# Kernel optimization log

Measured on AMD Instinct MI355X. Metric: run time of the kernel, lower is better.

The kernel has to match this reference:

```python
import jax, jax.numpy as jnp
import numpy as np

SL, BS, HS, FFN, E, TOPK = 2048, 4, 1024, 4096, 8, 2
T = SL * BS

def setup_inputs() -> dict:
    key = jax.random.key(0)
    k1, k2, k3, k4, k5, k6 = jax.random.split(key, 6)
    x = jax.random.normal(k1, (SL, BS, HS), dtype=jnp.float32)
    expert_weights = jax.random.uniform(k2, (T, TOPK), dtype=jnp.float32)
    expert_indices = jax.random.randint(k3, (T, TOPK), 0, E).astype(jnp.int64)
    scores = jax.random.uniform(k4, (T, TOPK), dtype=jnp.float32)
    w1 = jax.random.normal(k5, (E, HS, FFN), dtype=jnp.float32) * 0.02
    w2 = jax.random.normal(k6, (E, FFN, HS), dtype=jnp.float32) * 0.02
    return {"x": x, "expert_weights": expert_weights, "scores": scores,
            "w1": w1, "w2": w2, "expert_indices": expert_indices}

def reference(x, expert_weights, scores, w1, w2, expert_indices):
    # Dropless MoE dispatch-compute-combine with router_type=None.
    # Math identity: megablocks gather/grouped-GEMM/scatter with per-copy
    # expert_weights equals, for each token t:
    #   out[t] = sum_k expert_weights[t,k] * MLP_{e(t,k)}(x[t])
    # We fold the top-k copies into a per-(token, expert) combine weight and
    # run one GEMM pair per expert (fixed small E), matching the grouped GEMM.
    sl, bs, hs = x.shape
    num_experts = w1.shape[0]
    xf = x.reshape(-1, hs)  # [T, hs]
    onehot = jax.nn.one_hot(expert_indices, num_experts, dtype=x.dtype)  # [T, k, E]
    combine = jnp.einsum("tk,tke->et", expert_weights, onehot)  # [E, T]

    def expert_step(acc, inputs):
        w1e, w2e, cw = inputs  # [hs, ffn], [ffn, hs], [T]
        h = jax.nn.gelu(xf @ w1e, approximate=False)  # [T, ffn]
        acc = acc + cw[:, None] * (h @ w2e)  # [T, hs]
        return acc, None

    out, _ = jax.lax.scan(expert_step, jnp.zeros_like(xf), (w1, w2, combine))
    return out.reshape(sl, bs, hs)
```

## Files before the change

### kernel.cpp

```cpp
#include <hip/hip_runtime.h>
#include <hip/hip_bf16.h>
#include <math.h>
#include <stdint.h>

#define N_TOK   8192
#define HS      1024
#define FFN     4096
#define NE      8
#define NA      16384
#define CAP     16384
#define BM      256
#define MAXT    72

typedef __attribute__((ext_vector_type(8))) short          bf16x8;
typedef __attribute__((ext_vector_type(4))) float          f32x4;
typedef __attribute__((ext_vector_type(4))) float          fvec4;
typedef __attribute__((ext_vector_type(4))) unsigned short usvec4;

__device__ __forceinline__ void gl_lds16(const void* g, void* l) {
  __builtin_amdgcn_global_load_lds(
      (const __attribute__((address_space(1))) unsigned int*)g,
      (__attribute__((address_space(3))) unsigned int*)l,
      16, 0, 0);
}

__device__ __forceinline__ unsigned short f2bf(float f) {
  union { float f; unsigned int u; } v; v.f = f;
  unsigned int r = v.u + 0x7FFFu + ((v.u >> 16) & 1u);
  return (unsigned short)(r >> 16);
}


__global__ void cvt_x_kernel(const fvec4* __restrict__ in, unsigned short* __restrict__ out, int n4) {
  int i = blockIdx.x * 256 + threadIdx.x;
  if (i >= n4) return;
  fvec4 v = in[i];
  usvec4 o;
  o[0] = f2bf(v[0]); o[1] = f2bf(v[1]); o[2] = f2bf(v[2]); o[3] = f2bf(v[3]);
  *(usvec4*)(out + (size_t)i * 4) = o;
}

__global__ void tpose_cvt_kernel(const float* __restrict__ in, unsigned short* __restrict__ out,
                                 int R, int C) {
  __shared__ float t[64][65];
  int bc = blockIdx.x * 64, br = blockIdx.y * 64, e = blockIdx.z;
  const float* ine = in + (size_t)e * R * C;
  unsigned short* oute = out + (size_t)e * R * C;
  int tx = threadIdx.x & 63, ty = threadIdx.x >> 6;
#pragma unroll
  for (int q = 0; q < 16; ++q) {
    int r = ty * 16 + q;
    t[r][tx] = ine[(size_t)(br + r) * C + bc + tx];
  }
  __syncthreads();
#pragma unroll
  for (int q = 0; q < 16; ++q) {
    int c = ty * 16 + q;
    oute[(size_t)(bc + c) * R + br + tx] = f2bf(t[tx][c]);
  }
}


__global__ void route_kernel(const int* __restrict__ idx, const float* __restrict__ wts,
                             int* __restrict__ counts, int* __restrict__ btok,
                             int* __restrict__ bslot, float* __restrict__ bw) {
  int a = blockIdx.x * 256 + threadIdx.x;
  if (a >= NA) return;
  int e = idx[a];
  int pos = atomicAdd(&counts[e], 1);
  btok[(size_t)e * CAP + pos]  = a >> 1;
  bslot[(size_t)e * CAP + pos] = a;
  bw[(size_t)e * CAP + pos]    = wts[a];
}

__global__ void build_tiles_kernel(int* __restrict__ counts, int2* __restrict__ table) {
  if (threadIdx.x == 0 && blockIdx.x == 0) {
    int nt = 0;
    for (int e = 0; e < NE; ++e) {
      int c = counts[e];
      int t = (c + BM - 1) >> 8;
      for (int m = 0; m < t && nt < MAXT; ++m) table[nt++] = make_int2(e, m);
    }
    counts[8] = nt;
  }
}

template <int NWN, int EPI, int KDIM>
__global__ __launch_bounds__(NWN * 128, 2)
void moe_gemm(const unsigned short* __restrict__ Ab,
              const unsigned short* __restrict__ Bb,
              unsigned short* __restrict__ hout,
              float* __restrict__ perm,
              const int* __restrict__ btok,
              const int* __restrict__ bslot,
              const float* __restrict__ bw,
              const int* __restrict__ counts,
              const int2* __restrict__ table,
              int p0, int tc) {
  constexpr int NWAVES = 2 * NWN;
  constexpr int BN_ = NWN * 64;
  constexpr int NCH = 16 + BN_ / 16;
  constexpr int CPW = NCH / NWAVES;
  constexpr int BUFSZ = 16384 + BN_ * 64;
  constexpr int NT = KDIM / 32;

  __shared__ char lds[3 * BUFSZ];

  int nt = counts[8];
  int j = blockIdx.y;
  if (j < p0 || j >= p0 + tc || j >= nt) return;
  int2 te = table[j];
  int e = te.x, tm = te.y;
  int count = counts[e];
  int bn0 = blockIdx.x * BN_;
  int slotb = j - p0;

  int tid = threadIdx.x;
  int wid = tid >> 6, lane = tid & 63;
  int wm = wid / NWN, wn = wid % NWN;

  const unsigned short* Be = Bb + (size_t)e * ((size_t)FFN * HS);

  const char* src[CPW];
  int dst[CPW];
#pragma unroll
  for (int q = 0; q < CPW; ++q) {
    int c = wid * CPW + q;
    int rr = (c < 16 ? c * 16 : (c - 16) * 16) + (lane >> 2);
    int klog = ((lane & 3) * 16) ^ (((rr >> 1) & 3) << 4);
    if (c < 16) {
      dst[q] = c * 1024;
      if (EPI == 0) {
        int grow = tm * BM + rr;
        int tok = (grow < count) ? btok[(size_t)e * CAP + grow] : 0;
        src[q] = (const char*)(Ab + (size_t)tok * KDIM) + klog;
      } else {
        src[q] = (const char*)(Ab + ((size_t)slotb * BM + rr) * KDIM) + klog;
      }
    } else {
      dst[q] = 16384 + (c - 16) * 1024;
      src[q] = (const char*)(Be + (size_t)(bn0 + rr) * KDIM) + klog;
    }
  }

  int rA = wm * 128 + (lane & 15);
  int rB = wn * 64 + (lane & 15);
  int ks = (lane >> 4) * 16;
  int offA0 = rA * 64 + (ks ^ (((rA >> 1) & 3) << 4));
  int offB0 = 16384 + rB * 64 + (ks ^ (((rB >> 1) & 3) << 4));

  f32x4 acc[8][4] = {};

#pragma unroll
  for (int q = 0; q < CPW; ++q) gl_lds16(src[q], lds + dst[q]);
#pragma unroll
  for (int q = 0; q < CPW; ++q) gl_lds16(src[q] + 64, lds + BUFSZ + dst[q]);

  int bi = 0;
  for (int t = 0; t < NT; ++t) {
    if constexpr (CPW == 4) asm volatile("s_waitcnt vmcnt(4)" ::: "memory");
    else                    asm volatile("s_waitcnt vmcnt(6)" ::: "memory");
    __builtin_amdgcn_sched_barrier(0);
    __builtin_amdgcn_s_barrier();
    __builtin_amdgcn_sched_barrier(0);

    int kt2 = t + 2; if (kt2 >= NT) kt2 -= NT;
    int bi2 = bi + 2; if (bi2 >= 3) bi2 -= 3;
    char* db = lds + bi2 * BUFSZ;
#pragma unroll
    for (int q = 0; q < CPW; ++q)
      gl_lds16(src[q] + (size_t)kt2 * 64, db + dst[q]);

    const char* rbuf = lds + bi * BUFSZ;
    bf16x8 a[8], b[4];
#pragma unroll
    for (int i = 0; i < 8; ++i) a[i] = *(const bf16x8*)(rbuf + offA0 + i * 1024);
#pragma unroll
    for (int n = 0; n < 4; ++n) b[n] = *(const bf16x8*)(rbuf + offB0 + n * 1024);
    asm volatile("s_waitcnt lgkmcnt(0)" ::: "memory");
    __builtin_amdgcn_sched_barrier(0);
    __builtin_amdgcn_s_setprio(1);
#pragma unroll
    for (int i = 0; i < 8; ++i)
#pragma unroll
      for (int n = 0; n < 4; ++n)
        acc[i][n] = __builtin_amdgcn_mfma_f32_16x16x32_bf16(a[i], b[n], acc[i][n], 0, 0, 0);
    __builtin_amdgcn_s_setprio(0);
    ++bi; if (bi >= 3) bi = 0;
  }

  if (EPI == 0) {
    size_t hb = (size_t)slotb * BM;
#pragma unroll
    for (int i = 0; i < 8; ++i) {
      int row = wm * 128 + i * 16 + ((lane >> 4) << 2);
#pragma unroll
      for (int n = 0; n < 4; ++n) {
        int col = bn0 + wn * 64 + n * 16 + (lane & 15);
#pragma unroll
        for (int r = 0; r < 4; ++r) {
          float v = acc[i][n][r];
          float aa = fabsf(v) * 0.70710678118654752f;
          float tt = 1.0f / (1.0f + 0.3275911f * aa);
          float p = ((((1.061405429f * tt - 1.453152027f) * tt + 1.421413741f) * tt
                      - 0.284496736f) * tt + 0.254829592f) * tt;
          float er = 1.0f - p * __expf(-aa * aa);
          float g = 0.5f * v * (v >= 0.f ? (1.0f + er) : (1.0f - er));
          hout[(hb + row + r) * FFN + col] = f2bf(g);
        }
      }
    }
  } else {
#pragma unroll
    for (int i = 0; i < 8; ++i) {
      int rowb = wm * 128 + i * 16 + ((lane >> 4) << 2);
#pragma unroll
      for (int r = 0; r < 4; ++r) {
        int grow = tm * BM + rowb + r;
        if (grow < count) {
          int s = bslot[(size_t)e * CAP + grow];
          float wgt = bw[(size_t)e * CAP + grow];
#pragma unroll
          for (int n = 0; n < 4; ++n) {
            int col = bn0 + wn * 64 + n * 16 + (lane & 15);
            perm[(size_t)s * HS + col] = wgt * acc[i][n][r];
          }
        }
      }
    }
  }
}

__global__ void combine_kernel(const fvec4* __restrict__ perm, fvec4* __restrict__ out, int n4) {
  int i = blockIdx.x * 256 + threadIdx.x;
  if (i >= n4) return;
  int t = i >> 8;
  int c = i & 255;
  out[i] = perm[(size_t)(2 * t) * 256 + c] + perm[(size_t)(2 * t + 1) * 256 + c];
}


extern "C" void kernel_launch(void* const* d_in, const int* in_sizes, int n_in,
                              void* d_out, int out_size, void* d_ws, size_t ws_size,
                              hipStream_t stream) {
  const float* x   = (const float*)d_in[0];
  const float* ew  = (const float*)d_in[1];
  const float* w1  = (const float*)d_in[3];
  const float* w2  = (const float*)d_in[4];
  const int*   eix = (const int*)d_in[5];

  char* ws = (char*)d_ws;
  const size_t o_w1T    = 0;
  const size_t o_w2T    = 67108864ULL;
  const size_t o_xb     = 134217728ULL;
  const size_t o_btok   = 150994944ULL;
  const size_t o_bslot  = 151519232ULL;
  const size_t o_bw     = 152043520ULL;
  const size_t o_counts = 152567808ULL;
  const size_t o_table  = 152568064ULL;
  const size_t o_perm   = 152569344ULL;
  const size_t o_h      = 219678208ULL;

  unsigned short* w1T = (unsigned short*)(ws + o_w1T);
  unsigned short* w2T = (unsigned short*)(ws + o_w2T);
  unsigned short* xb  = (unsigned short*)(ws + o_xb);
  int*   btok   = (int*)(ws + o_btok);
  int*   bslot  = (int*)(ws + o_bslot);
  float* bw     = (float*)(ws + o_bw);
  int*   counts = (int*)(ws + o_counts);
  int2*  table  = (int2*)(ws + o_table);
  float* perm   = (float*)(ws + o_perm);
  unsigned short* hbuf = (unsigned short*)(ws + o_h);

  long long havail = (long long)ws_size - (long long)o_h;
  long long tile_bytes = (long long)BM * FFN * 2;
  int tc = (int)(havail / tile_bytes);
  if (tc < 1) tc = 1;
  if (tc > MAXT) tc = MAXT;
  int npass = (MAXT + tc - 1) / tc;

  hipMemsetAsync(counts, 0, 256, stream);

  cvt_x_kernel<<<(N_TOK * HS / 4 + 255) / 256, 256, 0, stream>>>(
      (const fvec4*)x, xb, N_TOK * HS / 4);
  tpose_cvt_kernel<<<dim3(FFN / 64, HS / 64, NE), 256, 0, stream>>>(w1, w1T, HS, FFN);
  tpose_cvt_kernel<<<dim3(HS / 64, FFN / 64, NE), 256, 0, stream>>>(w2, w2T, FFN, HS);

  route_kernel<<<(NA + 255) / 256, 256, 0, stream>>>(eix, ew, counts, btok, bslot, bw);
  build_tiles_kernel<<<1, 64, 0, stream>>>(counts, table);

  for (int p = 0; p < npass; ++p) {
    moe_gemm<4, 0, HS><<<dim3(FFN / 256, MAXT), 512, 0, stream>>>(
        xb, w1T, hbuf, perm, btok, bslot, bw, counts, table, p * tc, tc);
    moe_gemm<2, 1, FFN><<<dim3(HS / 128, MAXT), 256, 0, stream>>>(
        hbuf, w2T, hbuf, perm, btok, bslot, bw, counts, table, p * tc, tc);
  }

  combine_kernel<<<(N_TOK * HS / 4 + 255) / 256, 256, 0, stream>>>(
      (const fvec4*)perm, (fvec4*)d_out, N_TOK * HS / 4);
}
```

Baseline: 654.7 us.

## Remap GEMM grid for XCD-aware tile grouping, interleave LDS reads with MFMA, use tanh GELU

The block grid is flattened to 1D and remapped so that all N-blocks of the same M-tile land on the same XCD (bid&7). The aim is better L2 reuse of the A tile. The LDS fragment loads are split into groups separated by sched barriers, and the MFMA loop is chunked the same way, so LDS reads can overlap matrix ops instead of waiting on lgkmcnt(0). The erf-based GELU epilogue is replaced with a tanh approximation computed via exp. This is cheaper but numerically differs from exact GELU, which the reference uses.

```diff
diff --git a/kernel.cpp b/kernel.cpp
--- a/kernel.cpp
+++ b/kernel.cpp
@@ -85,7 +85,7 @@
   }
 }
 
-template <int NWN, int EPI, int KDIM>
+template <int NWN, int EPI, int KDIM, int NOUT>
 __global__ __launch_bounds__(NWN * 128, 2)
 void moe_gemm(const unsigned short* __restrict__ Ab,
               const unsigned short* __restrict__ Bb,
@@ -99,6 +99,7 @@
               int p0, int tc) {
   constexpr int NWAVES = 2 * NWN;
   constexpr int BN_ = NWN * 64;
+  constexpr int NBLK = NOUT / BN_;
   constexpr int NCH = 16 + BN_ / 16;
   constexpr int CPW = NCH / NWAVES;
   constexpr int BUFSZ = 16384 + BN_ * 64;
@@ -106,13 +107,16 @@
 
   __shared__ char lds[3 * BUFSZ];
 
+  int bid = blockIdx.x;
+  int xcd = bid & 7, slot = bid >> 3;
+  int j = xcd + 8 * (slot / NBLK);
+  int bn0 = (slot % NBLK) * BN_;
+
   int nt = counts[8];
-  int j = blockIdx.y;
   if (j < p0 || j >= p0 + tc || j >= nt) return;
   int2 te = table[j];
   int e = te.x, tm = te.y;
   int count = counts[e];
-  int bn0 = blockIdx.x * BN_;
   int slotb = j - p0;
 
   int tid = threadIdx.x;
@@ -173,18 +177,32 @@
 
     const char* rbuf = lds + bi * BUFSZ;
     bf16x8 a[8], b[4];
-#pragma unroll
-    for (int i = 0; i < 8; ++i) a[i] = *(const bf16x8*)(rbuf + offA0 + i * 1024);
-#pragma unroll
-    for (int n = 0; n < 4; ++n) b[n] = *(const bf16x8*)(rbuf + offB0 + n * 1024);
-    asm volatile("s_waitcnt lgkmcnt(0)" ::: "memory");
+    b[0] = *(const bf16x8*)(rbuf + offB0);
+    b[1] = *(const bf16x8*)(rbuf + offB0 + 1024);
+    b[2] = *(const bf16x8*)(rbuf + offB0 + 2048);
+    b[3] = *(const bf16x8*)(rbuf + offB0 + 3072);
+    a[0] = *(const bf16x8*)(rbuf + offA0);
+    a[1] = *(const bf16x8*)(rbuf + offA0 + 1024);
+    __builtin_amdgcn_sched_barrier(0);
+    a[2] = *(const bf16x8*)(rbuf + offA0 + 2048);
+    a[3] = *(const bf16x8*)(rbuf + offA0 + 3072);
+    __builtin_amdgcn_sched_barrier(0);
+    a[4] = *(const bf16x8*)(rbuf + offA0 + 4096);
+    a[5] = *(const bf16x8*)(rbuf + offA0 + 5120);
+    __builtin_amdgcn_sched_barrier(0);
+    a[6] = *(const bf16x8*)(rbuf + offA0 + 6144);
+    a[7] = *(const bf16x8*)(rbuf + offA0 + 7168);
     __builtin_amdgcn_sched_barrier(0);
     __builtin_amdgcn_s_setprio(1);
 #pragma unroll
-    for (int i = 0; i < 8; ++i)
-#pragma unroll
-      for (int n = 0; n < 4; ++n)
-        acc[i][n] = __builtin_amdgcn_mfma_f32_16x16x32_bf16(a[i], b[n], acc[i][n], 0, 0, 0);
+    for (int g = 0; g < 4; ++g) {
+#pragma unroll
+      for (int i = 2 * g; i < 2 * g + 2; ++i)
+#pragma unroll
+        for (int n = 0; n < 4; ++n)
+          acc[i][n] = __builtin_amdgcn_mfma_f32_16x16x32_bf16(a[i], b[n], acc[i][n], 0, 0, 0);
+      __builtin_amdgcn_sched_barrier(0);
+    }
     __builtin_amdgcn_s_setprio(0);
     ++bi; if (bi >= 3) bi = 0;
   }
@@ -200,12 +218,11 @@
 #pragma unroll
         for (int r = 0; r < 4; ++r) {
           float v = acc[i][n][r];
-          float aa = fabsf(v) * 0.70710678118654752f;
-          float tt = 1.0f / (1.0f + 0.3275911f * aa);
-          float p = ((((1.061405429f * tt - 1.453152027f) * tt + 1.421413741f) * tt
-                      - 0.284496736f) * tt + 0.254829592f) * tt;
-          float er = 1.0f - p * __expf(-aa * aa);
-          float g = 0.5f * v * (v >= 0.f ? (1.0f + er) : (1.0f - er));
+          float x2 = v * v;
+          float u2 = 1.5957691216057308f * v * fmaf(0.044715f, x2, 1.0f);
+          u2 = fminf(fmaxf(u2, -30.f), 30.f);
+          float ee = __expf(u2);
+          float g = v * __fdividef(ee, ee + 1.0f);
           hout[(hb + row + r) * FFN + col] = f2bf(g);
         }
       }
@@ -290,9 +307,9 @@
   build_tiles_kernel<<<1, 64, 0, stream>>>(counts, table);
 
   for (int p = 0; p < npass; ++p) {
-    moe_gemm<4, 0, HS><<<dim3(FFN / 256, MAXT), 512, 0, stream>>>(
+    moe_gemm<4, 0, HS, FFN><<<dim3(MAXT * 16), 512, 0, stream>>>(
         xb, w1T, hbuf, perm, btok, bslot, bw, counts, table, p * tc, tc);
-    moe_gemm<2, 1, FFN><<<dim3(HS / 128, MAXT), 256, 0, stream>>>(
+    moe_gemm<2, 1, FFN, HS><<<dim3(MAXT * 8), 256, 0, stream>>>(
         hbuf, w2T, hbuf, perm, btok, bslot, bw, counts, table, p * tc, tc);
   }
 
```

Result: faster. 608.4 us (-7.1%).
